# Kernel optimization log

Measured on AMD Instinct MI355X. Metric: run time of the kernel, lower is better.

The kernel has to match this reference:

```python
import jax, jax.numpy as jnp
import numpy as np

N = 100000      # nodes
D = 64          # feature dim (in_channels == out_channels)
K = 16          # num_neighbors -> E = N*(K-1) directed edges
NEG_SLOPE = 0.2 # GATConv negative_slope


def setup_inputs() -> dict:
    key = jax.random.key(0)
    k1, k2, k3, k4, k5 = jax.random.split(key, 5)
    E = N * (K - 1)
    x = jax.random.normal(k1, (N, D), dtype=jnp.float32)
    edge_index = jax.random.randint(k2, (2, E), 0, N, dtype=jnp.int32)
    W = jax.random.normal(k3, (D, D), dtype=jnp.float32) / np.sqrt(D).astype(np.float32)
    att_src = jax.random.normal(k4, (D,), dtype=jnp.float32) / np.sqrt(D).astype(np.float32)
    att_dst = jax.random.normal(k5, (D,), dtype=jnp.float32) / np.sqrt(D).astype(np.float32)
    bias = jnp.zeros((D,), dtype=jnp.float32)
    return {"x": x, "edge_index": edge_index, "W": W,
            "att_src": att_src, "att_dst": att_dst, "bias": bias}


def gat_forward(x, W, att_src, att_dst, bias, src, dst):
    # PyG GATConv, heads=1, concat=True, dropout=0, + outer ReLU from LNLE.forward
    h = x @ W                                   # [N, D] transformed nodes
    a_src = h @ att_src                         # [N] source attention logits
    a_dst = h @ att_dst                         # [N] target attention logits
    e = jax.nn.leaky_relu(a_src[src] + a_dst[dst], NEG_SLOPE)  # [E]
    # numerically-stable segment softmax over edges grouped by destination
    emax = jax.ops.segment_max(e, dst, num_segments=N)         # [N]
    p = jnp.exp(e - emax[dst])                                 # [E]
    psum = jax.ops.segment_sum(p, dst, num_segments=N)         # [N]
    alpha = p / (psum[dst] + jnp.float32(1e-16))               # [E]
    msg = h[src] * alpha[:, None]                              # [E, D] gather + weight
    out = jax.ops.segment_sum(msg, dst, num_segments=N) + bias # [N, D] scatter-add
    return jax.nn.relu(out)


def reference(x, edge_index, W, att_src, att_dst, bias):
    # GATConv default add_self_loops=True: append (i -> i) for every node
    loops = jnp.arange(N, dtype=edge_index.dtype)
    src = jnp.concatenate([edge_index[0], loops])   # message sources j
    dst = jnp.concatenate([edge_index[1], loops])   # message targets i
    return gat_forward(x, W, att_src, att_dst, bias, src, dst)
```

## Files before the change

kernel.cpp:

```cpp
#include <hip/hip_runtime.h>
#include <hip/hip_bf16.h>
#include <hip/hip_fp16.h>


#define GAT_N 100000
#define GAT_D 64
#define GAT_E 1500000
#define NEG_SLOPE 0.2f
#define NB ((GAT_N + 255) >> 8)
#define PC 3072
#define CAP_P 5120
#define CAP_C (CAP_P + 256)
#define RPAD 16
#define GPITCH 68
#define GEMM_BLKS ((GAT_N + 63) / 64)
#define PART_BLKS ((GAT_E + PC - 1) / PC)

__device__ __forceinline__ float lrelu(float e) {
    return e > 0.f ? e : NEG_SLOPE * e;
}

__global__ __launch_bounds__(256) void zinit_k(int* __restrict__ runctr) {
    const int i = blockIdx.x * 256 + threadIdx.x;
    if (i < NB) runctr[i * RPAD] = i * CAP_P;
}

__global__ __launch_bounds__(256, 4) void pg_k(
        const float* __restrict__ x, const float* __restrict__ W,
        const float* __restrict__ att_s, const float* __restrict__ att_d,
        unsigned* __restrict__ h, float* __restrict__ a_src, float* __restrict__ a_dst,
        const int* __restrict__ src, const int* __restrict__ dst,
        int* __restrict__ runctr, int* __restrict__ pairs) {
    __shared__ __align__(16) int smem[8448];
    const int t = threadIdx.x;

    if (blockIdx.x < GEMM_BLKS) {
        float* xl = (float*)smem;
        float* Wl = (float*)(smem + 4352);
        const int rowbase = blockIdx.x * 64;
        {
            const float4* W4 = (const float4*)W;
            float4* Wl4 = (float4*)Wl;
            #pragma unroll
            for (int i = 0; i < 4; ++i) Wl4[i * 256 + t] = W4[i * 256 + t];
        }
        #pragma unroll
        for (int i = 0; i < 4; ++i) {
            const int g = i * 256 + t;
            const int row = g >> 4, c4 = g & 15;
            float4 v = make_float4(0.f, 0.f, 0.f, 0.f);
            if (rowbase + row < GAT_N)
                v = ((const float4*)x)[(size_t)(rowbase + row) * 16 + c4];
            *(float4*)&xl[row * GPITCH + c4 * 4] = v;
        }
        __syncthreads();

        const int tx = t & 15, ty = t >> 4;
        float4 acc[4] = {};
        #pragma unroll 4
        for (int k0 = 0; k0 < GAT_D; k0 += 4) {
            const float4 w0 = *(const float4*)&Wl[(k0 + 0) * 64 + tx * 4];
            const float4 w1 = *(const float4*)&Wl[(k0 + 1) * 64 + tx * 4];
            const float4 w2 = *(const float4*)&Wl[(k0 + 2) * 64 + tx * 4];
            const float4 w3 = *(const float4*)&Wl[(k0 + 3) * 64 + tx * 4];
            #pragma unroll
            for (int i = 0; i < 4; ++i) {
                const float4 xv = *(const float4*)&xl[(ty * 4 + i) * GPITCH + k0];
                acc[i].x = fmaf(xv.x, w0.x, fmaf(xv.y, w1.x, fmaf(xv.z, w2.x, fmaf(xv.w, w3.x, acc[i].x))));
                acc[i].y = fmaf(xv.x, w0.y, fmaf(xv.y, w1.y, fmaf(xv.z, w2.y, fmaf(xv.w, w3.y, acc[i].y))));
                acc[i].z = fmaf(xv.x, w0.z, fmaf(xv.y, w1.z, fmaf(xv.z, w2.z, fmaf(xv.w, w3.z, acc[i].z))));
                acc[i].w = fmaf(xv.x, w0.w, fmaf(xv.y, w1.w, fmaf(xv.z, w2.w, fmaf(xv.w, w3.w, acc[i].w))));
            }
        }
        const float4 as4 = ((const float4*)att_s)[tx];
        const float4 ad4 = ((const float4*)att_d)[tx];
        #pragma unroll
        for (int i = 0; i < 4; ++i) {
            const int row = rowbase + ty * 4 + i;
            if (row < GAT_N) {
                const __half2 lo = __floats2half2_rn(acc[i].x, acc[i].y);
                const __half2 hi = __floats2half2_rn(acc[i].z, acc[i].w);
                ((uint2*)h)[(size_t)row * 16 + tx] =
                    make_uint2(*(const unsigned*)&lo, *(const unsigned*)&hi);
            }
            float ps = acc[i].x * as4.x + acc[i].y * as4.y + acc[i].z * as4.z + acc[i].w * as4.w;
            float pd = acc[i].x * ad4.x + acc[i].y * ad4.y + acc[i].z * ad4.z + acc[i].w * ad4.w;
            #pragma unroll
            for (int o = 8; o > 0; o >>= 1) {
                ps += __shfl_down(ps, o, 64);
                pd += __shfl_down(pd, o, 64);
            }
            if (tx == 0 && row < GAT_N) { a_src[row] = ps; a_dst[row] = pd; }
        }
    } else {
        int* lh    = smem;
        int* sc    = smem + 512;
        int* lb    = smem + 768;
        int* gpos  = smem + 1280;
        int* run   = smem + 1792;
        int* tgt   = smem + 2304;
        int* stage = smem + 5376;
        const int base = (blockIdx.x - GEMM_BLKS) * PC;

        lh[t] = 0; lh[t + 256] = 0;
        __syncthreads();
        for (int i = t; i < PC; i += 256) {
            const int e = base + i;
            if (e < GAT_E) atomicAdd(&lh[dst[e] >> 8], 1);
        }
        __syncthreads();
        const int a = lh[2 * t], b = lh[2 * t + 1];
        sc[t] = a + b; __syncthreads();
        for (int off = 1; off < 256; off <<= 1) {
            const int xch = (t >= off) ? sc[t - off] : 0;
            __syncthreads();
            sc[t] += xch;
            __syncthreads();
        }
        const int base0 = sc[t] - (a + b);
        lb[2 * t] = base0; lb[2 * t + 1] = base0 + a;
        #pragma unroll
        for (int k = 0; k < 2; ++k) {
            const int i = 2 * t + k;
            run[i] = lb[i];
            gpos[i] = (i < NB && lh[i]) ? atomicAdd(&runctr[i * RPAD], lh[i]) : 0;
        }
        __syncthreads();
        for (int i = t; i < PC; i += 256) {
            const int e = base + i;
            if (e < GAT_E) {
                const int sv = src[e], dv = dst[e];
                const int bk = dv >> 8;
                const int slot = atomicAdd(&run[bk], 1);
                stage[slot] = (sv << 8) | (dv & 255);
                tgt[slot] = gpos[bk] + (slot - lb[bk]);
            }
        }
        __syncthreads();
        const int cnt_total = min(PC, GAT_E - base);
        for (int i = t; i < cnt_total; i += 256) pairs[tgt[i]] = stage[i];
    }
}

__global__ __launch_bounds__(512) void csr_bucket_k(
        const int* __restrict__ pairs, const int* __restrict__ runctr,
        int* __restrict__ rowinfo, int* __restrict__ csr) {
    __shared__ int cnt[256], pfx[256];
    __shared__ int lcsr[CAP_C];
    const int b = blockIdx.x;
    const int t = threadIdx.x;
    const int node0 = b << 8;
    const int nnodes = min(256, GAT_N - node0);
    const int pbeg = b * CAP_P;
    const int ne = runctr[b * RPAD] - pbeg;
    const int cbase = b * CAP_C;

    if (t < 256) cnt[t] = (t < nnodes) ? 1 : 0;
    __syncthreads();
    for (int i = t; i < ne; i += 512)
        atomicAdd(&cnt[pairs[pbeg + i] & 255], 1);
    __syncthreads();
    if (t < 256) pfx[t] = cnt[t];
    __syncthreads();
    for (int off = 1; off < 256; off <<= 1) {
        const int x = (t < 256 && t >= off) ? pfx[t - off] : 0;
        __syncthreads();
        if (t < 256) pfx[t] += x;
        __syncthreads();
    }
    if (t < 256) {
        const int v = cnt[t];
        const int excl = pfx[t] - v;
        if (t < nnodes) {
            rowinfo[node0 + t] = ((cbase + excl) << 8) | v;
            lcsr[excl] = node0 + t;
        }
        cnt[t] = excl + ((t < nnodes) ? 1 : 0);
    }
    __syncthreads();
    for (int i = t; i < ne; i += 512) {
        const int p = pairs[pbeg + i];
        const int pos = atomicAdd(&cnt[p & 255], 1);
        lcsr[pos] = p >> 8;
    }
    __syncthreads();
    const int tot = ne + nnodes;
    for (int i = t; i < tot; i += 512) csr[cbase + i] = lcsr[i];
}

#define GATHER4(ACC, EIDX)                                              \
    {                                                                   \
        const float w_ = __shfl(alpha, (EIDX), 64);                     \
        const int   s_ = __shfl(s, (EIDX), 64);                         \
        const uint2 v_ = h2[(size_t)s_ * 16 + fl];                      \
        const float2 fa_ = __half22float2(*(const __half2*)&v_.x);      \
        const float2 fb_ = __half22float2(*(const __half2*)&v_.y);      \
        ACC.x = fmaf(w_, fa_.x, ACC.x);                                 \
        ACC.y = fmaf(w_, fa_.y, ACC.y);                                 \
        ACC.z = fmaf(w_, fb_.x, ACC.z);                                 \
        ACC.w = fmaf(w_, fb_.y, ACC.w);                                 \
    }

__device__ __noinline__ void gat_one_node(
        int d, int beg, int deg, int lane,
        const int* __restrict__ csr_src,
        const float* __restrict__ a_src, const float* __restrict__ a_dst,
        const unsigned* __restrict__ h, const float* __restrict__ bias,
        float* __restrict__ out) {
    const int end = beg + deg;
    const float ad = a_dst[d];
    if (deg <= 64) {
        const int k = beg + lane;
        const bool valid = k < end;
        const int s = valid ? csr_src[k] : 0;
        const float e = valid ? lrelu(a_src[s] + ad) : -3.4e38f;
        float m = e;
        #pragma unroll
        for (int o = 32; o > 0; o >>= 1) m = fmaxf(m, __shfl_down(m, o, 64));
        m = __shfl(m, 0, 64);
        const float p = valid ? __expf(e - m) : 0.f;
        float S = p;
        #pragma unroll
        for (int o = 32; o > 0; o >>= 1) S += __shfl_down(S, o, 64);
        S = __shfl(S, 0, 64);
        const float alpha = p / (S + 1e-16f);
        const int q = lane >> 4, fl = lane & 15;
        const uint2* __restrict__ h2 = (const uint2*)h;
        float4 A = {0,0,0,0}, B = {0,0,0,0}, C = {0,0,0,0}, D = {0,0,0,0};
        int j = 0;
        for (; j + 16 <= deg; j += 16) {
            GATHER4(A, j + q);
            GATHER4(B, j + 4 + q);
            GATHER4(C, j + 8 + q);
            GATHER4(D, j + 12 + q);
        }
        if (j < deg)      GATHER4(A, j + q);
        if (j + 4 < deg)  GATHER4(B, j + 4 + q);
        if (j + 8 < deg)  GATHER4(C, j + 8 + q);
        if (j + 12 < deg) GATHER4(D, j + 12 + q);
        float4 acc;
        acc.x = (A.x + B.x) + (C.x + D.x);
        acc.y = (A.y + B.y) + (C.y + D.y);
        acc.z = (A.z + B.z) + (C.z + D.z);
        acc.w = (A.w + B.w) + (C.w + D.w);
        acc.x += __shfl_xor(acc.x, 16, 64); acc.x += __shfl_xor(acc.x, 32, 64);
        acc.y += __shfl_xor(acc.y, 16, 64); acc.y += __shfl_xor(acc.y, 32, 64);
        acc.z += __shfl_xor(acc.z, 16, 64); acc.z += __shfl_xor(acc.z, 32, 64);
        acc.w += __shfl_xor(acc.w, 16, 64); acc.w += __shfl_xor(acc.w, 32, 64);
        if (q == 0) {
            const float4 bi = ((const float4*)bias)[fl];
            float4 o;
            o.x = fmaxf(acc.x + bi.x, 0.f);
            o.y = fmaxf(acc.y + bi.y, 0.f);
            o.z = fmaxf(acc.z + bi.z, 0.f);
            o.w = fmaxf(acc.w + bi.w, 0.f);
            ((float4*)out)[(size_t)d * 16 + fl] = o;
        }
    } else {
        float m = -3.4e38f;
        for (int base = beg; base < end; base += 64) {
            const int k = base + lane;
            if (k < end) m = fmaxf(m, lrelu(a_src[csr_src[k]] + ad));
        }
        #pragma unroll
        for (int o = 32; o > 0; o >>= 1) m = fmaxf(m, __shfl_down(m, o, 64));
        m = __shfl(m, 0, 64);
        float S = 0.f;
        for (int base = beg; base < end; base += 64) {
            const int k = base + lane;
            if (k < end) S += __expf(lrelu(a_src[csr_src[k]] + ad) - m);
        }
        #pragma unroll
        for (int o = 32; o > 0; o >>= 1) S += __shfl_down(S, o, 64);
        S = __shfl(S, 0, 64);
        const float inv = 1.f / (S + 1e-16f);
        float acc = 0.f;
        const unsigned short* hb = (const unsigned short*)h;
        for (int base = beg; base < end; base += 64) {
            const int k = base + lane;
            int s = 0; float alpha = 0.f;
            if (k < end) {
                s = csr_src[k];
                alpha = __expf(lrelu(a_src[s] + ad) - m) * inv;
            }
            const int lim = min(64, end - base);
            for (int j2 = 0; j2 < lim; ++j2) {
                const float aj = __shfl(alpha, j2, 64);
                const int   sj = __shfl(s, j2, 64);
                const unsigned short u = hb[(size_t)sj * 64 + lane];
                acc = fmaf(aj, __half2float(*(const __half*)&u), acc);
            }
        }
        const float v = acc + bias[lane];
        out[(size_t)d * GAT_D + lane] = v > 0.f ? v : 0.f;
    }
}

__global__ __launch_bounds__(256) void gat_node_k(
        const int* __restrict__ rowinfo, const int* __restrict__ csr_src,
        const float* __restrict__ a_src, const float* __restrict__ a_dst,
        const unsigned* __restrict__ h, const float* __restrict__ bias,
        float* __restrict__ out) {
    const int pair = blockIdx.x * 4 + (threadIdx.x >> 6);
    const int lane = threadIdx.x & 63;
    const int half = lane >> 5, l32 = lane & 31;
    const int n0 = pair * 2;
    const int n = n0 + half;

    const int ri  = rowinfo[n];
    const int beg = ri >> 8;
    const int deg = ri & 255;
    const int dm  = max(deg, __shfl_xor(deg, 32, 64));

    if (dm <= 31) {
        const float ad = a_dst[n];
        const bool valid = l32 < deg;
        const int k = beg + l32;
        const int s = valid ? csr_src[k] : 0;
        const float e0 = valid ? lrelu(a_src[s] + ad) : -3.4e38f;
        float m = e0;
        #pragma unroll
        for (int o = 16; o > 0; o >>= 1) m = fmaxf(m, __shfl_xor(m, o, 64));
        const float p = valid ? __expf(e0 - m) : 0.f;
        float S = p;
        #pragma unroll
        for (int o = 16; o > 0; o >>= 1) S += __shfl_xor(S, o, 64);
        const float alpha = p / (S + 1e-16f);

        const int sub = (lane >> 4) & 1, fl = lane & 15;
        const int hb5 = lane & 32;
        const uint2* __restrict__ h2 = (const uint2*)h;
        float4 A = {0,0,0,0}, B = {0,0,0,0}, C = {0,0,0,0}, D = {0,0,0,0};
        int j = 0;
        for (; j + 8 <= dm; j += 8) {
            GATHER4(A, hb5 + j + sub);
            GATHER4(B, hb5 + j + 2 + sub);
            GATHER4(C, hb5 + j + 4 + sub);
            GATHER4(D, hb5 + j + 6 + sub);
        }
        if (j < dm)     GATHER4(A, hb5 + j + sub);
        if (j + 2 < dm) GATHER4(B, hb5 + j + 2 + sub);
        if (j + 4 < dm) GATHER4(C, hb5 + j + 4 + sub);
        if (j + 6 < dm) GATHER4(D, hb5 + j + 6 + sub);

        float4 acc;
        acc.x = (A.x + B.x) + (C.x + D.x);
        acc.y = (A.y + B.y) + (C.y + D.y);
        acc.z = (A.z + B.z) + (C.z + D.z);
        acc.w = (A.w + B.w) + (C.w + D.w);
        acc.x += __shfl_xor(acc.x, 16, 64);
        acc.y += __shfl_xor(acc.y, 16, 64);
        acc.z += __shfl_xor(acc.z, 16, 64);
        acc.w += __shfl_xor(acc.w, 16, 64);
        if (sub == 0) {
            const float4 bi = ((const float4*)bias)[fl];
            float4 o;
            o.x = fmaxf(acc.x + bi.x, 0.f);
            o.y = fmaxf(acc.y + bi.y, 0.f);
            o.z = fmaxf(acc.z + bi.z, 0.f);
            o.w = fmaxf(acc.w + bi.w, 0.f);
            ((float4*)out)[(size_t)n * 16 + fl] = o;
        }
    } else {
        const int ri0 = rowinfo[n0];
        gat_one_node(n0, ri0 >> 8, ri0 & 255, lane, csr_src, a_src, a_dst, h, bias, out);
        const int ri1 = rowinfo[n0 + 1];
        gat_one_node(n0 + 1, ri1 >> 8, ri1 & 255, lane, csr_src, a_src, a_dst, h, bias, out);
    }
}

extern "C" void kernel_launch(void* const* d_in, const int* in_sizes, int n_in,
                              void* d_out, int out_size, void* d_ws, size_t ws_size,
                              hipStream_t stream) {
    const float* x     = (const float*)d_in[0];
    const int*   ei    = (const int*)  d_in[1];
    const float* W     = (const float*)d_in[2];
    const float* att_s = (const float*)d_in[3];
    const float* att_d = (const float*)d_in[4];
    const float* bias  = (const float*)d_in[5];
    float* out = (float*)d_out;

    unsigned* h      = (unsigned*)d_ws;
    float*  a_src    = (float*)(h + (size_t)GAT_N * 32);
    float*  a_dst    = a_src + GAT_N;
    int*    pairs    = (int*)(a_dst + GAT_N);
    int*    runctr   = pairs + (size_t)NB * CAP_P;
    int*    rowinfo  = runctr + (size_t)NB * RPAD;
    int*    csr      = rowinfo + GAT_N;

    const int* src = ei;
    const int* dst = ei + GAT_E;

    zinit_k<<<2, 256, 0, stream>>>(runctr);
    pg_k<<<GEMM_BLKS + PART_BLKS, 256, 0, stream>>>(
        x, W, att_s, att_d, h, a_src, a_dst, src, dst, runctr, pairs);
    csr_bucket_k<<<NB, 512, 0, stream>>>(pairs, runctr, rowinfo, csr);
    gat_node_k<<<GAT_N / 8, 256, 0, stream>>>(rowinfo, csr, a_src, a_dst, h, bias, out);
}
```

Measured before the change: 171.7 us.

## Compute edge softmax in CSR bucket kernel and store packed (src, alpha) pairs

Moves the per-destination segment softmax (leaky-relu logits, max, exp, normalize) from the aggregation kernel into the CSR bucketing kernel, using shared memory per 256-node bucket. Edges are then written as packed (src index, alpha) uint2 pairs, so the aggregation kernel no longer does random a_src gathers or shuffle reductions. In exchange, CSR storage doubles in size, the bucket kernel now does the a_src gathers with extra shared memory (which may lower occupancy), and the softmax uses only two threads per row.

Result: slower. 182.3 us (+6.2%).

```diff
diff --git a/kernel.cpp b/kernel.cpp
--- a/kernel.cpp
+++ b/kernel.cpp
@@ -144,9 +144,12 @@
 
 __global__ __launch_bounds__(512) void csr_bucket_k(
         const int* __restrict__ pairs, const int* __restrict__ runctr,
-        int* __restrict__ rowinfo, int* __restrict__ csr) {
+        const float* __restrict__ a_src, const float* __restrict__ a_dst,
+        int* __restrict__ rowinfo, uint2* __restrict__ csrp) {
     __shared__ int cnt[256], pfx[256];
     __shared__ int lcsr[CAP_C];
+    __shared__ float le[CAP_C];
+    __shared__ float red[512];
     const int b = blockIdx.x;
     const int t = threadIdx.x;
     const int node0 = b << 8;
@@ -174,18 +177,44 @@
         if (t < nnodes) {
             rowinfo[node0 + t] = ((cbase + excl) << 8) | v;
             lcsr[excl] = node0 + t;
+            le[excl] = lrelu(a_src[node0 + t] + a_dst[node0 + t]);
         }
         cnt[t] = excl + ((t < nnodes) ? 1 : 0);
+        pfx[t] = excl;
     }
     __syncthreads();
     for (int i = t; i < ne; i += 512) {
         const int p = pairs[pbeg + i];
-        const int pos = atomicAdd(&cnt[p & 255], 1);
-        lcsr[pos] = p >> 8;
-    }
+        const int d8 = p & 255;
+        const int sv = p >> 8;
+        const int pos = atomicAdd(&cnt[d8], 1);
+        lcsr[pos] = sv;
+        le[pos] = lrelu(a_src[sv] + a_dst[node0 + d8]);
+    }
+    __syncthreads();
+    const int r = t & 255, hh = t >> 8;
+    int rbeg = 0, rdeg = 0;
+    if (r < nnodes) { rbeg = pfx[r]; rdeg = cnt[r] - rbeg; }
+    float m = -3.4e38f;
+    for (int k = hh; k < rdeg; k += 2) m = fmaxf(m, le[rbeg + k]);
+    red[t] = m;
+    __syncthreads();
+    m = fmaxf(red[r], red[r + 256]);
+    float S = 0.f;
+    for (int k = hh; k < rdeg; k += 2) {
+        const float p = __expf(le[rbeg + k] - m);
+        le[rbeg + k] = p;
+        S += p;
+    }
+    __syncthreads();
+    red[t] = S;
+    __syncthreads();
+    const float inv = 1.f / (red[r] + red[r + 256] + 1e-16f);
+    for (int k = hh; k < rdeg; k += 2) le[rbeg + k] *= inv;
     __syncthreads();
     const int tot = ne + nnodes;
-    for (int i = t; i < tot; i += 512) csr[cbase + i] = lcsr[i];
+    for (int i = t; i < tot; i += 512)
+        csrp[cbase + i] = make_uint2((unsigned)lcsr[i], __float_as_uint(le[i]));
 }
 
 #define GATHER4(ACC, EIDX)                                              \
@@ -203,27 +232,15 @@
 
 __device__ __noinline__ void gat_one_node(
         int d, int beg, int deg, int lane,
-        const int* __restrict__ csr_src,
-        const float* __restrict__ a_src, const float* __restrict__ a_dst,
+        const uint2* __restrict__ csrp,
         const unsigned* __restrict__ h, const float* __restrict__ bias,
         float* __restrict__ out) {
-    const int end = beg + deg;
-    const float ad = a_dst[d];
     if (deg <= 64) {
-        const int k = beg + lane;
-        const bool valid = k < end;
-        const int s = valid ? csr_src[k] : 0;
-        const float e = valid ? lrelu(a_src[s] + ad) : -3.4e38f;
-        float m = e;
-        #pragma unroll
-        for (int o = 32; o > 0; o >>= 1) m = fmaxf(m, __shfl_down(m, o, 64));
-        m = __shfl(m, 0, 64);
-        const float p = valid ? __expf(e - m) : 0.f;
-        float S = p;
-        #pragma unroll
-        for (int o = 32; o > 0; o >>= 1) S += __shfl_down(S, o, 64);
-        S = __shfl(S, 0, 64);
-        const float alpha = p / (S + 1e-16f);
+        const bool valid = lane < deg;
+        uint2 pk = make_uint2(0u, 0u);
+        if (valid) pk = csrp[beg + lane];
+        const int s = (int)pk.x;
+        const float alpha = __uint_as_float(pk.y);
         const int q = lane >> 4, fl = lane & 15;
         const uint2* __restrict__ h2 = (const uint2*)h;
         float4 A = {0,0,0,0}, B = {0,0,0,0}, C = {0,0,0,0}, D = {0,0,0,0};
@@ -257,31 +274,16 @@
             ((float4*)out)[(size_t)d * 16 + fl] = o;
         }
     } else {
-        float m = -3.4e38f;
-        for (int base = beg; base < end; base += 64) {
-            const int k = base + lane;
-            if (k < end) m = fmaxf(m, lrelu(a_src[csr_src[k]] + ad));
-        }
-        #pragma unroll
-        for (int o = 32; o > 0; o >>= 1) m = fmaxf(m, __shfl_down(m, o, 64));
-        m = __shfl(m, 0, 64);
-        float S = 0.f;
-        for (int base = beg; base < end; base += 64) {
-            const int k = base + lane;
-            if (k < end) S += __expf(lrelu(a_src[csr_src[k]] + ad) - m);
-        }
-        #pragma unroll
-        for (int o = 32; o > 0; o >>= 1) S += __shfl_down(S, o, 64);
-        S = __shfl(S, 0, 64);
-        const float inv = 1.f / (S + 1e-16f);
         float acc = 0.f;
         const unsigned short* hb = (const unsigned short*)h;
+        const int end = beg + deg;
         for (int base = beg; base < end; base += 64) {
             const int k = base + lane;
             int s = 0; float alpha = 0.f;
             if (k < end) {
-                s = csr_src[k];
-                alpha = __expf(lrelu(a_src[s] + ad) - m) * inv;
+                const uint2 pk = csrp[k];
+                s = (int)pk.x;
+                alpha = __uint_as_float(pk.y);
             }
             const int lim = min(64, end - base);
             for (int j2 = 0; j2 < lim; ++j2) {
@@ -297,8 +299,7 @@
 }
 
 __global__ __launch_bounds__(256) void gat_node_k(
-        const int* __restrict__ rowinfo, const int* __restrict__ csr_src,
-        const float* __restrict__ a_src, const float* __restrict__ a_dst,
+        const int* __restrict__ rowinfo, const uint2* __restrict__ csrp,
         const unsigned* __restrict__ h, const float* __restrict__ bias,
         float* __restrict__ out) {
     const int pair = blockIdx.x * 4 + (threadIdx.x >> 6);
@@ -313,19 +314,11 @@
     const int dm  = max(deg, __shfl_xor(deg, 32, 64));
 
     if (dm <= 31) {
-        const float ad = a_dst[n];
         const bool valid = l32 < deg;
-        const int k = beg + l32;
-        const int s = valid ? csr_src[k] : 0;
-        const float e0 = valid ? lrelu(a_src[s] + ad) : -3.4e38f;
-        float m = e0;
-        #pragma unroll
-        for (int o = 16; o > 0; o >>= 1) m = fmaxf(m, __shfl_xor(m, o, 64));
-        const float p = valid ? __expf(e0 - m) : 0.f;
-        float S = p;
-        #pragma unroll
-        for (int o = 16; o > 0; o >>= 1) S += __shfl_xor(S, o, 64);
-        const float alpha = p / (S + 1e-16f);
+        uint2 pk = make_uint2(0u, 0u);
+        if (valid) pk = csrp[beg + l32];
+        const int s = (int)pk.x;
+        const float alpha = __uint_as_float(pk.y);
 
         const int sub = (lane >> 4) & 1, fl = lane & 15;
         const int hb5 = lane & 32;
@@ -363,9 +356,9 @@
         }
     } else {
         const int ri0 = rowinfo[n0];
-        gat_one_node(n0, ri0 >> 8, ri0 & 255, lane, csr_src, a_src, a_dst, h, bias, out);
+        gat_one_node(n0, ri0 >> 8, ri0 & 255, lane, csrp, h, bias, out);
         const int ri1 = rowinfo[n0 + 1];
-        gat_one_node(n0 + 1, ri1 >> 8, ri1 & 255, lane, csr_src, a_src, a_dst, h, bias, out);
+        gat_one_node(n0 + 1, ri1 >> 8, ri1 & 255, lane, csrp, h, bias, out);
     }
 }
 
@@ -386,7 +379,7 @@
     int*    pairs    = (int*)(a_dst + GAT_N);
     int*    runctr   = pairs + (size_t)NB * CAP_P;
     int*    rowinfo  = runctr + (size_t)NB * RPAD;
-    int*    csr      = rowinfo + GAT_N;
+    uint2*  csrp     = (uint2*)(rowinfo + GAT_N);
 
     const int* src = ei;
     const int* dst = ei + GAT_E;
@@ -394,6 +387,6 @@
     zinit_k<<<2, 256, 0, stream>>>(runctr);
     pg_k<<<GEMM_BLKS + PART_BLKS, 256, 0, stream>>>(
         x, W, att_s, att_d, h, a_src, a_dst, src, dst, runctr, pairs);
-    csr_bucket_k<<<NB, 512, 0, stream>>>(pairs, runctr, rowinfo, csr);
-    gat_node_k<<<GAT_N / 8, 256, 0, stream>>>(rowinfo, csr, a_src, a_dst, h, bias, out);
-}
+    csr_bucket_k<<<NB, 512, 0, stream>>>(pairs, runctr, a_src, a_dst, rowinfo, csrp);
+    gat_node_k<<<GAT_N / 8, 256, 0, stream>>>(rowinfo, csrp, h, bias, out);
+}
```
